# Kernel tuning notes

Hardware: AMD Instinct MI355X
Metric: run time of the kernel (lower is better)

Reference implementation:

```python
import jax, jax.numpy as jnp
import numpy as np

D = 128          # node_embed_size
N_NODES = 100000
E = 600000       # edges per relation (3 relations)
NEG_SLOPE = 0.01 # F.leaky_relu default


def setup_inputs() -> dict:
    key = jax.random.key(0)
    ks = jax.random.split(key, 17)
    s = 1.0 / np.sqrt(D)
    inp = {
        "N": jax.random.normal(ks[0], (N_NODES, D), jnp.float32),
        # fc1 weights per domain: [D, D] (torch Linear weight layout: out x in)
        "W1_0": jax.random.normal(ks[1], (D, D), jnp.float32) * s,
        "W1_1": jax.random.normal(ks[2], (D, D), jnp.float32) * s,
        "W1_2": jax.random.normal(ks[3], (D, D), jnp.float32) * s,
        # fc2 weights per domain: [1, 2D]
        "w2_0": jax.random.normal(ks[4], (1, 2 * D), jnp.float32) * s,
        "w2_1": jax.random.normal(ks[5], (1, 2 * D), jnp.float32) * s,
        "w2_2": jax.random.normal(ks[6], (1, 2 * D), jnp.float32) * s,
        "Wq": jax.random.normal(ks[7], (D, D), jnp.float32) * s,
        "Wk": jax.random.normal(ks[8], (D, D), jnp.float32) * s,
        "Wv": jax.random.normal(ks[9], (D, D), jnp.float32) * s,
        "src0": jax.random.randint(ks[10], (E,), 0, N_NODES, jnp.int32),
        "dst0": jax.random.randint(ks[11], (E,), 0, N_NODES, jnp.int32),
        "src1": jax.random.randint(ks[12], (E,), 0, N_NODES, jnp.int32),
        "dst1": jax.random.randint(ks[13], (E,), 0, N_NODES, jnp.int32),
        "src2": jax.random.randint(ks[14], (E,), 0, N_NODES, jnp.int32),
        "dst2": jax.random.randint(ks[15], (E,), 0, N_NODES, jnp.int32),
        "target_idx": 0,
    }
    return inp


def _leaky(x):
    return jnp.where(x >= 0, x, NEG_SLOPE * x)


def _gat_relation(N, W1, w2, src, dst, n_nodes):
    # e_edge = leaky_relu(fc2(cat(fc1(N[src]), fc1(N[dst]))))
    # fc2 on a concat == left half dot src part + right half dot dst part,
    # so compute per-node scores once and gather (standard GAT trick).
    d = N.shape[1]
    h = N @ W1.T                      # [n, d]
    sl = h @ w2[0, :d]                # [n]
    sr = h @ w2[0, d:]                # [n]
    e = _leaky(sl[src] + sr[dst])     # [E]
    # segment softmax over edges grouped by destination node (DGL mailbox softmax)
    m = jax.ops.segment_max(e, dst, num_segments=n_nodes)   # [n], -inf for empty
    ex = jnp.exp(e - m[dst])                                 # [E]
    den = jax.ops.segment_sum(ex, dst, num_segments=n_nodes) # [n]
    alpha = ex / den[dst]                                    # [E]
    # weighted sum of source features; zero for nodes with no in-edges
    return jax.ops.segment_sum(alpha[:, None] * N[src], dst, num_segments=n_nodes)


def reference(N, W1_0, W1_1, W1_2, w2_0, w2_1, w2_2, Wq, Wk, Wv,
              src0, dst0, src1, dst1, src2, dst2, target_idx):
    n, d = N.shape
    rels = [(W1_0, w2_0, src0, dst0), (W1_1, w2_1, src1, dst1), (W1_2, w2_2, src2, dst2)]
    h = [_gat_relation(N, W1, w2, src, dst, n) for (W1, w2, src, dst) in rels]
    hs = jnp.stack(h)                         # [3, n, d]
    q = h[target_idx] @ Wq.T                  # [n, d]
    k = jnp.einsum('knd,ed->kne', hs, Wk)     # [3, n, d]
    # (Wv value is computed in the original but never used in the output)
    e = jnp.einsum('nd,knd->nk', q, k) / jnp.sqrt(jnp.asarray(d, N.dtype))  # [n, 3]
    a = jax.nn.softmax(e, axis=1)             # [n, 3]
    Np = jnp.einsum('nk,knd->nd', a, hs)      # [n, d]
    return Np
```

## Files before the change

kernel.cpp:

```cpp
#include <hip/hip_runtime.h>
#include <hip/hip_bf16.h>
#include <math.h>

#define DD 128

typedef __attribute__((ext_vector_type(8))) short short8;
typedef __attribute__((ext_vector_type(4))) float f32x4;

static __device__ __forceinline__ unsigned short f2bf(float f) {
    unsigned u = __float_as_uint(f);
    u += 0x7fffu + ((u >> 16) & 1u);
    return (unsigned short)(u >> 16);
}
static __device__ __forceinline__ float bflo(unsigned mm) { return __uint_as_float(mm << 16); }
static __device__ __forceinline__ float bfhi(unsigned mm) { return __uint_as_float(mm & 0xffff0000u); }

static __device__ __forceinline__ f32x4 MFMA(short8 a, short8 b, f32x4 c) {
    return __builtin_amdgcn_mfma_f32_16x16x32_bf16(a, b, c, 0, 0, 0);
}
static __device__ __forceinline__ int uswz(int u) { return u ^ ((u >> 4) & 7); }

__global__ void k_fill(float* __restrict__ out, float v, int n) {
    int i = blockIdx.x * 256 + threadIdx.x;
    if (i < n) out[i] = v;
}

__global__ void k_prep(const float* __restrict__ Wq, const float* __restrict__ Wk,
                       const float* __restrict__ W10, const float* __restrict__ W11,
                       const float* __restrict__ W12,
                       const float* __restrict__ w20, const float* __restrict__ w21,
                       const float* __restrict__ w22,
                       unsigned short* __restrict__ Bh, unsigned short* __restrict__ Bl,
                       float* __restrict__ uv, unsigned* __restrict__ cnt, int SEG) {
    int b = blockIdx.x, j = threadIdx.x;
    if (b < DD) {
        float acc = 0.f;
        for (int k = 0; k < DD; ++k)
            acc += Wq[k*DD + b] * Wk[k*DD + j];
        unsigned short hi = f2bf(acc);
        unsigned short lo = f2bf(acc - bflo(hi));
        int t  = j >> 4;
        int ks = b >> 5;
        int l  = ((b >> 3) & 3) * 16 + (j & 15);
        int jj = b & 7;
        int idx = ((t*4 + ks)*64 + l)*8 + jj;
        Bh[idx] = hi;
        Bl[idx] = lo;
    } else if (b < DD + 3) {
        int r = b - DD;
        const float* W1 = (r==0) ? W10 : (r==1 ? W11 : W12);
        const float* w2 = (r==0) ? w20 : (r==1 ? w21 : w22);
        float u = 0.f, v = 0.f;
        for (int k = 0; k < DD; ++k) {
            float w = W1[k*DD + j];
            u += w2[k]      * w;
            v += w2[DD + k] * w;
        }
        uv[r*256 + j]      = u;
        uv[r*256 + DD + j] = v;
    } else {
        int idx = (b - (DD + 3)) * DD + j;
        if (idx < SEG) cnt[idx] = 0u;
    }
}

__global__ void __launch_bounds__(256) k_scores(
        const float* __restrict__ N, const float* __restrict__ uv,
        float* __restrict__ sl, float* __restrict__ sr,
        uint2* __restrict__ Nbf, unsigned* __restrict__ cnt,
        unsigned* __restrict__ rank,
        const int* __restrict__ d0, const int* __restrict__ d1,
        const int* __restrict__ d2,
        int n, int E) {
    int tid = threadIdx.x;
    int g = blockIdx.x * 256 + tid;
    if (g < 3*E) {
        int r = (g >= 2*E) ? 2 : (g >= E ? 1 : 0);
        int e = g - r*E;
        const int* Dd = (r==0) ? d0 : (r==1 ? d1 : d2);
        rank[g] = atomicAdd(&cnt[(size_t)r*n + Dd[e]], 1u);
    }
    int wave = tid >> 6, lane = tid & 63, half = lane >> 5, l32 = lane & 31;
    int iw = blockIdx.x * 8 + wave * 2 + half;
    if (iw >= n && blockIdx.x * 8 >= n) return;
    int i = (iw < n) ? iw : (n - 1);
    float4 nv = ((const float4*)N)[(size_t)i * 32 + l32];
    if (iw < n) {
        uint2 pk;
        pk.x = (unsigned)f2bf(nv.x) | ((unsigned)f2bf(nv.y) << 16);
        pk.y = (unsigned)f2bf(nv.z) | ((unsigned)f2bf(nv.w) << 16);
        Nbf[(size_t)iw * 32 + l32] = pk;
    }
    const float4* UV4 = (const float4*)uv;
    float acc[6];
#pragma unroll
    for (int r = 0; r < 3; ++r) {
        float4 u = UV4[r*64 + l32];
        float4 v = UV4[r*64 + 32 + l32];
        acc[2*r]   = nv.x*u.x + nv.y*u.y + nv.z*u.z + nv.w*u.w;
        acc[2*r+1] = nv.x*v.x + nv.y*v.y + nv.z*v.z + nv.w*v.w;
    }
#pragma unroll
    for (int o = 16; o; o >>= 1) {
#pragma unroll
        for (int q = 0; q < 6; ++q) acc[q] += __shfl_xor(acc[q], o);
    }
    if (l32 == 0 && iw < n) {
#pragma unroll
        for (int r = 0; r < 3; ++r) {
            sl[(size_t)r*n + iw] = acc[2*r];
            sr[(size_t)r*n + iw] = acc[2*r+1];
        }
    }
}

__global__ void __launch_bounds__(256) k_scan1(unsigned* __restrict__ off,
                                               unsigned* __restrict__ bsum, int SEG) {
    __shared__ unsigned s[256];
    int tid = threadIdx.x;
    int i = blockIdx.x * 256 + tid;
    unsigned v = (i < SEG) ? off[i] : 0u;
    s[tid] = v; __syncthreads();
#pragma unroll
    for (int o = 1; o < 256; o <<= 1) {
        unsigned a = (tid >= o) ? s[tid - o] : 0u; __syncthreads();
        s[tid] += a; __syncthreads();
    }
    if (i < SEG) off[i] = s[tid] - v;
    if (tid == 255) bsum[blockIdx.x] = s[255];
}

__global__ void __launch_bounds__(256) k_scan2(unsigned* __restrict__ bsum, int nb) {
    __shared__ unsigned s[256];
    __shared__ unsigned carry;
    int tid = threadIdx.x;
    if (tid == 0) carry = 0u;
    for (int base = 0; base < nb; base += 256) {
        int i = base + tid;
        unsigned v = (i < nb) ? bsum[i] : 0u;
        __syncthreads();
        s[tid] = v; __syncthreads();
#pragma unroll
        for (int o = 1; o < 256; o <<= 1) {
            unsigned a = (tid >= o) ? s[tid - o] : 0u; __syncthreads();
            s[tid] += a; __syncthreads();
        }
        unsigned incl = s[tid], tot = s[255], c = carry;
        if (i < nb) bsum[i] = c + incl - v;
        __syncthreads();
        if (tid == 0) carry = c + tot;
    }
}

__global__ void k_scatter(const int* __restrict__ s0, const int* __restrict__ d0,
                          const int* __restrict__ s1, const int* __restrict__ d1,
                          const int* __restrict__ s2, const int* __restrict__ d2,
                          const float* __restrict__ sl, const float* __restrict__ sr,
                          const unsigned* __restrict__ off,
                          const unsigned* __restrict__ bsum,
                          const unsigned* __restrict__ rank,
                          uint2* __restrict__ edat, int n, int E) {
    int g = blockIdx.x * 256 + threadIdx.x;
    if (g >= 3*E) return;
    int r = (g >= 2*E) ? 2 : (g >= E ? 1 : 0);
    int e = g - r*E;
    const int* S  = (r==0) ? s0 : (r==1 ? s1 : s2);
    const int* Dd = (r==0) ? d0 : (r==1 ? d1 : d2);
    int si = S[e], di = Dd[e];
    int seg = r*n + di;
    float x = sl[(size_t)r*n + si] + sr[seg];
    x = (x >= 0.f) ? x : 0.01f * x;
    unsigned p = off[seg] + bsum[seg >> 8] + rank[g];
    edat[p] = make_uint2((unsigned)si, __float_as_uint(x));
}

__global__ void __launch_bounds__(256, 8) k_node(
        const uint4* __restrict__ Nbf,
        const uint4* __restrict__ B4h, const uint4* __restrict__ B4l,
        const unsigned* __restrict__ off,
        const unsigned* __restrict__ bsum,
        const uint2* __restrict__ edat,
        const int* __restrict__ tgt,
        float* __restrict__ out, int n, int TOT) {
    __shared__ uint4 afrag[2][256];
    __shared__ float Tl[16*132];
    int tid = threadIdx.x;
    int wave = tid >> 6, lane = tid & 63;
    int grp = lane >> 4;
    int l16 = lane & 15;
    int nid = wave * 4 + grp;
    int iw = blockIdx.x * 16 + nid;
    int i = (iw < n) ? iw : (n - 1);
    int t = tgt[0];
    t = (t < 0) ? 0 : (t > 2 ? 2 : t);
    int SEG = 3*n;

    int A[3], C[3];
#pragma unroll
    for (int r = 0; r < 3; ++r) {
        int seg = r*n + i;
        int a = (int)(off[seg] + bsum[seg >> 8]);
        int b = (seg + 1 < SEG) ? (int)(off[seg+1] + bsum[(seg+1) >> 8]) : TOT;
        A[r] = a; C[r] = b - a;
    }

    float m_[3], inv_[3];
#pragma unroll
    for (int r = 0; r < 3; ++r) {
        int cc = C[r];
        float m, s;
        if (cc <= 16) {
            float x = (l16 < cc) ? __uint_as_float(edat[A[r] + l16].y) : -INFINITY;
            m = x;
#pragma unroll
            for (int o = 8; o; o >>= 1) m = fmaxf(m, __shfl_xor(m, o));
            s = (l16 < cc) ? __expf(x - m) : 0.f;
#pragma unroll
            for (int o = 8; o; o >>= 1) s += __shfl_xor(s, o);
        } else {
            m = -INFINITY;
            for (int j = A[r] + l16; j < A[r] + cc; j += 16)
                m = fmaxf(m, __uint_as_float(edat[j].y));
#pragma unroll
            for (int o = 8; o; o >>= 1) m = fmaxf(m, __shfl_xor(m, o));
            s = 0.f;
            for (int j = A[r] + l16; j < A[r] + cc; j += 16)
                s += __expf(__uint_as_float(edat[j].y) - m);
#pragma unroll
            for (int o = 8; o; o >>= 1) s += __shfl_xor(s, o);
        }
        m_[r] = m; inv_[r] = 1.f / s;
    }

    float hr[3][8];
#pragma unroll
    for (int r = 0; r < 3; ++r) {
        float h[8] = {0.f,0.f,0.f,0.f,0.f,0.f,0.f,0.f};
        int cc = C[r], a = A[r];
        float mm = m_[r], iv = inv_[r];
        for (int p = 0; p < cc; p += 2) {
            int e1 = (p + 1 < cc) ? p + 1 : cc - 1;
            uint2 d0 = edat[a + p];
            uint2 d1 = edat[a + e1];
            uint4 v0 = Nbf[(size_t)d0.x * 16 + l16];
            uint4 v1 = Nbf[(size_t)d1.x * 16 + l16];
            float a0 = __expf(__uint_as_float(d0.y) - mm) * iv;
            float a1 = (p + 1 < cc)
                ? __expf(__uint_as_float(d1.y) - mm) * iv : 0.f;
            h[0] += a0*bflo(v0.x) + a1*bflo(v1.x);
            h[1] += a0*bfhi(v0.x) + a1*bfhi(v1.x);
            h[2] += a0*bflo(v0.y) + a1*bflo(v1.y);
            h[3] += a0*bfhi(v0.y) + a1*bfhi(v1.y);
            h[4] += a0*bflo(v0.z) + a1*bflo(v1.z);
            h[5] += a0*bfhi(v0.z) + a1*bfhi(v1.z);
            h[6] += a0*bflo(v0.w) + a1*bflo(v1.w);
            h[7] += a0*bfhi(v0.w) + a1*bfhi(v1.w);
        }
#pragma unroll
        for (int k = 0; k < 8; ++k) hr[r][k] = h[k];
        if (r == t) {
            unsigned ph[4], pl[4];
#pragma unroll
            for (int k = 0; k < 4; ++k) {
                unsigned short h0 = f2bf(h[2*k]);
                unsigned short h1 = f2bf(h[2*k+1]);
                unsigned short g0 = f2bf(h[2*k]   - bflo(h0));
                unsigned short g1 = f2bf(h[2*k+1] - bflo(h1));
                ph[k] = (unsigned)h0 | ((unsigned)h1 << 16);
                pl[k] = (unsigned)g0 | ((unsigned)g1 << 16);
            }
            int u = uswz(((l16 >> 2) * 64) + ((l16 & 3) * 16) + nid);
            afrag[0][u] = make_uint4(ph[0], ph[1], ph[2], ph[3]);
            afrag[1][u] = make_uint4(pl[0], pl[1], pl[2], pl[3]);
        }
    }
    __syncthreads();

    {
        int qm = lane >> 4;
        f32x4 acc0 = {0.f, 0.f, 0.f, 0.f};
        f32x4 acc1 = {0.f, 0.f, 0.f, 0.f};
        int jt0 = wave*2, jt1 = wave*2 + 1;
        for (int ks = 0; ks < 4; ++ks) {
            uint4 a_hi = afrag[0][uswz(ks*64 + lane)];
            uint4 a_lo = afrag[1][uswz(ks*64 + lane)];
            uint4 b0h = B4h[(jt0*4 + ks)*64 + lane];
            uint4 b0l = B4l[(jt0*4 + ks)*64 + lane];
            uint4 b1h = B4h[(jt1*4 + ks)*64 + lane];
            uint4 b1l = B4l[(jt1*4 + ks)*64 + lane];
            acc0 = MFMA(__builtin_bit_cast(short8, a_hi),
                        __builtin_bit_cast(short8, b0h), acc0);
            acc1 = MFMA(__builtin_bit_cast(short8, a_hi),
                        __builtin_bit_cast(short8, b1h), acc1);
            acc0 = MFMA(__builtin_bit_cast(short8, a_lo),
                        __builtin_bit_cast(short8, b0h), acc0);
            acc1 = MFMA(__builtin_bit_cast(short8, a_lo),
                        __builtin_bit_cast(short8, b1h), acc1);
            acc0 = MFMA(__builtin_bit_cast(short8, a_hi),
                        __builtin_bit_cast(short8, b0l), acc0);
            acc1 = MFMA(__builtin_bit_cast(short8, a_hi),
                        __builtin_bit_cast(short8, b1l), acc1);
        }
        int col0 = jt0*16 + l16, col1 = jt1*16 + l16;
#pragma unroll
        for (int rg = 0; rg < 4; ++rg) {
            Tl[(qm*4 + rg)*132 + col0] = acc0[rg];
            Tl[(qm*4 + rg)*132 + col1] = acc1[rg];
        }
    }
    __syncthreads();

    float4 ta = *(const float4*)&Tl[nid*132 + 8*l16];
    float4 tb = *(const float4*)&Tl[nid*132 + 8*l16 + 4];
    float t8[8] = {ta.x, ta.y, ta.z, ta.w, tb.x, tb.y, tb.z, tb.w};

    const float inv = 0.088388347648318447f;
    float e[3];
#pragma unroll
    for (int r = 0; r < 3; ++r) {
        float v = 0.f;
#pragma unroll
        for (int k = 0; k < 8; ++k) v += t8[k]*hr[r][k];
#pragma unroll
        for (int o = 8; o; o >>= 1) v += __shfl_xor(v, o);
        e[r] = v * inv;
    }
    float mx = fmaxf(e[0], fmaxf(e[1], e[2]));
    float x0 = __expf(e[0]-mx), x1 = __expf(e[1]-mx), x2 = __expf(e[2]-mx);
    float sinv = 1.f / (x0 + x1 + x2);
    float aw0 = x0*sinv, aw1 = x1*sinv, aw2 = x2*sinv;
    if (iw < n) {
        float4 oa, ob;
        oa.x = aw0*hr[0][0] + aw1*hr[1][0] + aw2*hr[2][0];
        oa.y = aw0*hr[0][1] + aw1*hr[1][1] + aw2*hr[2][1];
        oa.z = aw0*hr[0][2] + aw1*hr[1][2] + aw2*hr[2][2];
        oa.w = aw0*hr[0][3] + aw1*hr[1][3] + aw2*hr[2][3];
        ob.x = aw0*hr[0][4] + aw1*hr[1][4] + aw2*hr[2][4];
        ob.y = aw0*hr[0][5] + aw1*hr[1][5] + aw2*hr[2][5];
        ob.z = aw0*hr[0][6] + aw1*hr[1][6] + aw2*hr[2][6];
        ob.w = aw0*hr[0][7] + aw1*hr[1][7] + aw2*hr[2][7];
        ((float4*)(out + (size_t)iw * DD))[2*l16]     = oa;
        ((float4*)(out + (size_t)iw * DD))[2*l16 + 1] = ob;
    }
}

extern "C" void kernel_launch(void* const* d_in, const int* in_sizes, int n_in,
                              void* d_out, int out_size, void* d_ws, size_t ws_size,
                              hipStream_t stream) {
    float* outp = (float*)d_out;
    int fillgrid = (out_size + 255) / 256;
    if (n_in != 17) {
        k_fill<<<fillgrid, 256, 0, stream>>>(outp, 1024.0f, out_size);
        return;
    }
    int n = in_sizes[0] / DD;
    int E = in_sizes[10];
    bool ok = (in_sizes[0] % DD == 0)
        && in_sizes[1]==DD*DD && in_sizes[2]==DD*DD && in_sizes[3]==DD*DD
        && in_sizes[4]==2*DD  && in_sizes[5]==2*DD  && in_sizes[6]==2*DD
        && in_sizes[7]==DD*DD && in_sizes[8]==DD*DD && in_sizes[9]==DD*DD
        && in_sizes[11]==E && in_sizes[12]==E && in_sizes[13]==E
        && in_sizes[14]==E && in_sizes[15]==E && in_sizes[16]==1;
    if (!ok) {
        k_fill<<<fillgrid, 256, 0, stream>>>(outp, 512.0f, out_size);
        return;
    }
    int SEG = 3*n;
    int NB1 = (SEG + 255) / 256;
    int tot = 3*E;

    size_t o_edat = (size_t)2*SEG + 768 + DD*DD + SEG + NB1 + (size_t)tot;
    o_edat = (o_edat + 1) & ~(size_t)1;
    size_t o_nbf = o_edat + (size_t)2*tot;
    o_nbf = (o_nbf + 3) & ~(size_t)3;
    size_t need_f = o_nbf + (size_t)n*64;
    if (ws_size < need_f * sizeof(float)) {
        k_fill<<<fillgrid, 256, 0, stream>>>(outp, 256.0f, out_size);
        return;
    }

    const float* N   = (const float*)d_in[0];
    const float* W10 = (const float*)d_in[1];
    const float* W11 = (const float*)d_in[2];
    const float* W12 = (const float*)d_in[3];
    const float* w20 = (const float*)d_in[4];
    const float* w21 = (const float*)d_in[5];
    const float* w22 = (const float*)d_in[6];
    const float* Wq  = (const float*)d_in[7];
    const float* Wk  = (const float*)d_in[8];
    const int* s0 = (const int*)d_in[10];
    const int* d0 = (const int*)d_in[11];
    const int* s1 = (const int*)d_in[12];
    const int* d1 = (const int*)d_in[13];
    const int* s2 = (const int*)d_in[14];
    const int* d2 = (const int*)d_in[15];
    const int* tgt = (const int*)d_in[16];

    float* ws = (float*)d_ws;
    float* sl = ws;
    float* sr = sl + SEG;
    float* uv = sr + SEG;
    unsigned short* Bh = (unsigned short*)(uv + 768);
    unsigned short* Bl = Bh + DD*DD;
    unsigned* off  = (unsigned*)(uv + 768 + DD*DD);
    unsigned* bsum = off + SEG;
    unsigned* rank = bsum + NB1;
    uint2*    edat = (uint2*)(ws + o_edat);
    unsigned* Nbf  = (unsigned*)(ws + o_nbf);

    int NBZ = (SEG + DD - 1) / DD;
    int gridS = (n + 7) / 8;
    int gridC = (tot + 255) / 256;
    if (gridC > gridS) gridS = gridC;

    k_prep<<<DD + 3 + NBZ, DD, 0, stream>>>(Wq, Wk, W10, W11, W12,
                                            w20, w21, w22, Bh, Bl, uv, off, SEG);
    k_scores<<<gridS, 256, 0, stream>>>(N, uv, sl, sr, (uint2*)Nbf, off, rank,
                                        d0, d1, d2, n, E);
    k_scan1<<<NB1, 256, 0, stream>>>(off, bsum, SEG);
    k_scan2<<<1, 256, 0, stream>>>(bsum, NB1);
    k_scatter<<<(tot + 255)/256, 256, 0, stream>>>(s0,d0,s1,d1,s2,d2, sl,sr,
                                                   off, bsum, rank, edat, n, E);
    k_node<<<(n + 15)/16, 256, 0, stream>>>((const uint4*)Nbf,
                                            (const uint4*)Bh, (const uint4*)Bl,
                                            off, bsum, edat, tgt, outp, n, tot);
}
```

Measured before the change: 388.1 us.

## Fuse front-end kernels into one cooperative persistent kernel with grid syncs

Replaces the five front-end launches (prep, scores/counting, two scan passes, scatter) with a single cooperative kernel of 1024 blocks that uses grid-stride loops and grid-wide syncs between phases. This removes per-launch overhead and the pipeline drain between small kernels. In exchange, the grid barriers and the single-block second scan serialise work, and the fixed grid may underuse or oversubscribe the device. Cooperative launch also requires every block to be co-resident, with occupancy limited by launch_bounds(256,4).

```diff
diff --git a/kernel.cpp b/kernel.cpp
--- a/kernel.cpp
+++ b/kernel.cpp
@@ -1,8 +1,11 @@
 #include <hip/hip_runtime.h>
 #include <hip/hip_bf16.h>
+#include <hip/hip_cooperative_groups.h>
 #include <math.h>
 
 #define DD 128
+
+namespace cg = cooperative_groups;
 
 typedef __attribute__((ext_vector_type(8))) short short8;
 typedef __attribute__((ext_vector_type(4))) float f32x4;
@@ -25,29 +28,48 @@
     if (i < n) out[i] = v;
 }
 
-__global__ void k_prep(const float* __restrict__ Wq, const float* __restrict__ Wk,
-                       const float* __restrict__ W10, const float* __restrict__ W11,
-                       const float* __restrict__ W12,
-                       const float* __restrict__ w20, const float* __restrict__ w21,
-                       const float* __restrict__ w22,
-                       unsigned short* __restrict__ Bh, unsigned short* __restrict__ Bl,
-                       float* __restrict__ uv, unsigned* __restrict__ cnt, int SEG) {
-    int b = blockIdx.x, j = threadIdx.x;
-    if (b < DD) {
+__global__ void __launch_bounds__(256, 4) k_front(
+        const float* __restrict__ N,
+        const float* __restrict__ Wq, const float* __restrict__ Wk,
+        const float* __restrict__ W10, const float* __restrict__ W11,
+        const float* __restrict__ W12,
+        const float* __restrict__ w20, const float* __restrict__ w21,
+        const float* __restrict__ w22,
+        const int* __restrict__ s0, const int* __restrict__ d0,
+        const int* __restrict__ s1, const int* __restrict__ d1,
+        const int* __restrict__ s2, const int* __restrict__ d2,
+        unsigned short* __restrict__ Bh, unsigned short* __restrict__ Bl,
+        float* __restrict__ uv, float* __restrict__ sl, float* __restrict__ sr,
+        uint2* __restrict__ Nbf, unsigned* __restrict__ off,
+        unsigned* __restrict__ bsum, unsigned* __restrict__ rank,
+        uint2* __restrict__ edat,
+        int n, int E) {
+    cg::grid_group gg = cg::this_grid();
+    __shared__ unsigned smem[256];
+    __shared__ unsigned carry;
+    int tid = threadIdx.x, bid = blockIdx.x, nb = gridDim.x;
+    int gsz = nb * 256, g0 = bid * 256 + tid;
+    int SEG = 3*n;
+    int NB1 = (SEG + 255) >> 8;
+    int tot3 = 3*E;
+
+    for (int idx = g0; idx < DD*DD; idx += gsz) {
+        int c = idx >> 7, j = idx & 127;
         float acc = 0.f;
         for (int k = 0; k < DD; ++k)
-            acc += Wq[k*DD + b] * Wk[k*DD + j];
+            acc += Wq[k*DD + c] * Wk[k*DD + j];
         unsigned short hi = f2bf(acc);
         unsigned short lo = f2bf(acc - bflo(hi));
         int t  = j >> 4;
-        int ks = b >> 5;
-        int l  = ((b >> 3) & 3) * 16 + (j & 15);
-        int jj = b & 7;
-        int idx = ((t*4 + ks)*64 + l)*8 + jj;
-        Bh[idx] = hi;
-        Bl[idx] = lo;
-    } else if (b < DD + 3) {
-        int r = b - DD;
+        int ks = c >> 5;
+        int l  = ((c >> 3) & 3) * 16 + (j & 15);
+        int jj = c & 7;
+        int fidx = ((t*4 + ks)*64 + l)*8 + jj;
+        Bh[fidx] = hi;
+        Bl[fidx] = lo;
+    }
+    for (int idx = g0; idx < 3*DD; idx += gsz) {
+        int r = idx >> 7, j = idx & 127;
         const float* W1 = (r==0) ? W10 : (r==1 ? W11 : W12);
         const float* w2 = (r==0) ? w20 : (r==1 ? w21 : w22);
         float u = 0.f, v = 0.f;
@@ -58,120 +80,101 @@
         }
         uv[r*256 + j]      = u;
         uv[r*256 + DD + j] = v;
-    } else {
-        int idx = (b - (DD + 3)) * DD + j;
-        if (idx < SEG) cnt[idx] = 0u;
-    }
-}
-
-__global__ void __launch_bounds__(256) k_scores(
-        const float* __restrict__ N, const float* __restrict__ uv,
-        float* __restrict__ sl, float* __restrict__ sr,
-        uint2* __restrict__ Nbf, unsigned* __restrict__ cnt,
-        unsigned* __restrict__ rank,
-        const int* __restrict__ d0, const int* __restrict__ d1,
-        const int* __restrict__ d2,
-        int n, int E) {
-    int tid = threadIdx.x;
-    int g = blockIdx.x * 256 + tid;
-    if (g < 3*E) {
+    }
+    for (int idx = g0; idx < SEG; idx += gsz) off[idx] = 0u;
+    gg.sync();
+
+    for (int g = g0; g < tot3; g += gsz) {
         int r = (g >= 2*E) ? 2 : (g >= E ? 1 : 0);
         int e = g - r*E;
         const int* Dd = (r==0) ? d0 : (r==1 ? d1 : d2);
-        rank[g] = atomicAdd(&cnt[(size_t)r*n + Dd[e]], 1u);
-    }
-    int wave = tid >> 6, lane = tid & 63, half = lane >> 5, l32 = lane & 31;
-    int iw = blockIdx.x * 8 + wave * 2 + half;
-    if (iw >= n && blockIdx.x * 8 >= n) return;
-    int i = (iw < n) ? iw : (n - 1);
-    float4 nv = ((const float4*)N)[(size_t)i * 32 + l32];
-    if (iw < n) {
-        uint2 pk;
-        pk.x = (unsigned)f2bf(nv.x) | ((unsigned)f2bf(nv.y) << 16);
-        pk.y = (unsigned)f2bf(nv.z) | ((unsigned)f2bf(nv.w) << 16);
-        Nbf[(size_t)iw * 32 + l32] = pk;
-    }
-    const float4* UV4 = (const float4*)uv;
-    float acc[6];
-#pragma unroll
-    for (int r = 0; r < 3; ++r) {
-        float4 u = UV4[r*64 + l32];
-        float4 v = UV4[r*64 + 32 + l32];
-        acc[2*r]   = nv.x*u.x + nv.y*u.y + nv.z*u.z + nv.w*u.w;
-        acc[2*r+1] = nv.x*v.x + nv.y*v.y + nv.z*v.z + nv.w*v.w;
-    }
-#pragma unroll
-    for (int o = 16; o; o >>= 1) {
-#pragma unroll
-        for (int q = 0; q < 6; ++q) acc[q] += __shfl_xor(acc[q], o);
-    }
-    if (l32 == 0 && iw < n) {
-#pragma unroll
-        for (int r = 0; r < 3; ++r) {
-            sl[(size_t)r*n + iw] = acc[2*r];
-            sr[(size_t)r*n + iw] = acc[2*r+1];
-        }
-    }
-}
-
-__global__ void __launch_bounds__(256) k_scan1(unsigned* __restrict__ off,
-                                               unsigned* __restrict__ bsum, int SEG) {
-    __shared__ unsigned s[256];
-    int tid = threadIdx.x;
-    int i = blockIdx.x * 256 + tid;
-    unsigned v = (i < SEG) ? off[i] : 0u;
-    s[tid] = v; __syncthreads();
-#pragma unroll
-    for (int o = 1; o < 256; o <<= 1) {
-        unsigned a = (tid >= o) ? s[tid - o] : 0u; __syncthreads();
-        s[tid] += a; __syncthreads();
-    }
-    if (i < SEG) off[i] = s[tid] - v;
-    if (tid == 255) bsum[blockIdx.x] = s[255];
-}
-
-__global__ void __launch_bounds__(256) k_scan2(unsigned* __restrict__ bsum, int nb) {
-    __shared__ unsigned s[256];
-    __shared__ unsigned carry;
-    int tid = threadIdx.x;
-    if (tid == 0) carry = 0u;
-    for (int base = 0; base < nb; base += 256) {
-        int i = base + tid;
-        unsigned v = (i < nb) ? bsum[i] : 0u;
+        rank[g] = atomicAdd(&off[(size_t)r*n + Dd[e]], 1u);
+    }
+    {
+        int wave = tid >> 6, lane = tid & 63, half = lane >> 5, l32 = lane & 31;
+        int ntile = (n + 7) >> 3;
+        const float4* UV4 = (const float4*)uv;
+        for (int ib = bid; ib < ntile; ib += nb) {
+            int iw = ib*8 + wave*2 + half;
+            int i = (iw < n) ? iw : (n - 1);
+            float4 nv = ((const float4*)N)[(size_t)i * 32 + l32];
+            if (iw < n) {
+                uint2 pk;
+                pk.x = (unsigned)f2bf(nv.x) | ((unsigned)f2bf(nv.y) << 16);
+                pk.y = (unsigned)f2bf(nv.z) | ((unsigned)f2bf(nv.w) << 16);
+                Nbf[(size_t)iw * 32 + l32] = pk;
+            }
+            float acc[6];
+#pragma unroll
+            for (int r = 0; r < 3; ++r) {
+                float4 u = UV4[r*64 + l32];
+                float4 v = UV4[r*64 + 32 + l32];
+                acc[2*r]   = nv.x*u.x + nv.y*u.y + nv.z*u.z + nv.w*u.w;
+                acc[2*r+1] = nv.x*v.x + nv.y*v.y + nv.z*v.z + nv.w*v.w;
+            }
+#pragma unroll
+            for (int o = 16; o; o >>= 1) {
+#pragma unroll
+                for (int q = 0; q < 6; ++q) acc[q] += __shfl_xor(acc[q], o);
+            }
+            if (l32 == 0 && iw < n) {
+#pragma unroll
+                for (int r = 0; r < 3; ++r) {
+                    sl[(size_t)r*n + iw] = acc[2*r];
+                    sr[(size_t)r*n + iw] = acc[2*r+1];
+                }
+            }
+        }
+    }
+    gg.sync();
+
+    for (int tb = bid; tb < NB1; tb += nb) {
+        int i = tb*256 + tid;
+        unsigned v = (i < SEG) ? off[i] : 0u;
+        smem[tid] = v; __syncthreads();
+#pragma unroll
+        for (int o = 1; o < 256; o <<= 1) {
+            unsigned a = (tid >= o) ? smem[tid - o] : 0u; __syncthreads();
+            smem[tid] += a; __syncthreads();
+        }
+        if (i < SEG) off[i] = smem[tid] - v;
+        if (tid == 255) bsum[tb] = smem[255];
         __syncthreads();
-        s[tid] = v; __syncthreads();
-#pragma unroll
-        for (int o = 1; o < 256; o <<= 1) {
-            unsigned a = (tid >= o) ? s[tid - o] : 0u; __syncthreads();
-            s[tid] += a; __syncthreads();
-        }
-        unsigned incl = s[tid], tot = s[255], c = carry;
-        if (i < nb) bsum[i] = c + incl - v;
-        __syncthreads();
-        if (tid == 0) carry = c + tot;
-    }
-}
-
-__global__ void k_scatter(const int* __restrict__ s0, const int* __restrict__ d0,
-                          const int* __restrict__ s1, const int* __restrict__ d1,
-                          const int* __restrict__ s2, const int* __restrict__ d2,
-                          const float* __restrict__ sl, const float* __restrict__ sr,
-                          const unsigned* __restrict__ off,
-                          const unsigned* __restrict__ bsum,
-                          const unsigned* __restrict__ rank,
-                          uint2* __restrict__ edat, int n, int E) {
-    int g = blockIdx.x * 256 + threadIdx.x;
-    if (g >= 3*E) return;
-    int r = (g >= 2*E) ? 2 : (g >= E ? 1 : 0);
-    int e = g - r*E;
-    const int* S  = (r==0) ? s0 : (r==1 ? s1 : s2);
-    const int* Dd = (r==0) ? d0 : (r==1 ? d1 : d2);
-    int si = S[e], di = Dd[e];
-    int seg = r*n + di;
-    float x = sl[(size_t)r*n + si] + sr[seg];
-    x = (x >= 0.f) ? x : 0.01f * x;
-    unsigned p = off[seg] + bsum[seg >> 8] + rank[g];
-    edat[p] = make_uint2((unsigned)si, __float_as_uint(x));
+    }
+    gg.sync();
+
+    if (bid == 0) {
+        if (tid == 0) carry = 0u;
+        for (int base = 0; base < NB1; base += 256) {
+            int i = base + tid;
+            unsigned v = (i < NB1) ? bsum[i] : 0u;
+            __syncthreads();
+            smem[tid] = v; __syncthreads();
+#pragma unroll
+            for (int o = 1; o < 256; o <<= 1) {
+                unsigned a = (tid >= o) ? smem[tid - o] : 0u; __syncthreads();
+                smem[tid] += a; __syncthreads();
+            }
+            unsigned incl = smem[tid], tt = smem[255], c = carry;
+            if (i < NB1) bsum[i] = c + incl - v;
+            __syncthreads();
+            if (tid == 0) carry = c + tt;
+        }
+    }
+    gg.sync();
+
+    for (int g = g0; g < tot3; g += gsz) {
+        int r = (g >= 2*E) ? 2 : (g >= E ? 1 : 0);
+        int e = g - r*E;
+        const int* S  = (r==0) ? s0 : (r==1 ? s1 : s2);
+        const int* Dd = (r==0) ? d0 : (r==1 ? d1 : d2);
+        int si = S[e], di = Dd[e];
+        int seg = r*n + di;
+        float x = sl[(size_t)r*n + si] + sr[seg];
+        x = (x >= 0.f) ? x : 0.01f * x;
+        unsigned p = off[seg] + bsum[seg >> 8] + rank[g];
+        edat[p] = make_uint2((unsigned)si, __float_as_uint(x));
+    }
 }
 
 __global__ void __launch_bounds__(256, 8) k_node(
@@ -406,21 +409,23 @@
     unsigned* bsum = off + SEG;
     unsigned* rank = bsum + NB1;
     uint2*    edat = (uint2*)(ws + o_edat);
-    unsigned* Nbf  = (unsigned*)(ws + o_nbf);
-
-    int NBZ = (SEG + DD - 1) / DD;
-    int gridS = (n + 7) / 8;
-    int gridC = (tot + 255) / 256;
-    if (gridC > gridS) gridS = gridC;
-
-    k_prep<<<DD + 3 + NBZ, DD, 0, stream>>>(Wq, Wk, W10, W11, W12,
-                                            w20, w21, w22, Bh, Bl, uv, off, SEG);
-    k_scores<<<gridS, 256, 0, stream>>>(N, uv, sl, sr, (uint2*)Nbf, off, rank,
-                                        d0, d1, d2, n, E);
-    k_scan1<<<NB1, 256, 0, stream>>>(off, bsum, SEG);
-    k_scan2<<<1, 256, 0, stream>>>(bsum, NB1);
-    k_scatter<<<(tot + 255)/256, 256, 0, stream>>>(s0,d0,s1,d1,s2,d2, sl,sr,
-                                                   off, bsum, rank, edat, n, E);
+    uint2*    Nbf  = (uint2*)(ws + o_nbf);
+
+    {
+        int nn = n, EE = E;
+        void* args[] = {
+            (void*)&N, (void*)&Wq, (void*)&Wk,
+            (void*)&W10, (void*)&W11, (void*)&W12,
+            (void*)&w20, (void*)&w21, (void*)&w22,
+            (void*)&s0, (void*)&d0, (void*)&s1, (void*)&d1,
+            (void*)&s2, (void*)&d2,
+            (void*)&Bh, (void*)&Bl, (void*)&uv, (void*)&sl, (void*)&sr,
+            (void*)&Nbf, (void*)&off, (void*)&bsum, (void*)&rank,
+            (void*)&edat, (void*)&nn, (void*)&EE
+        };
+        hipLaunchCooperativeKernel((void*)k_front, dim3(1024), dim3(256),
+                                   args, 0, stream);
+    }
     k_node<<<(n + 15)/16, 256, 0, stream>>>((const uint4*)Nbf,
                                             (const uint4*)Bh, (const uint4*)Bl,
                                             off, bsum, edat, tgt, outp, n, tot);
```

Result: slower. 828.3 us (+113.4%).

## Replace two-pass scan with single-pass decoupled look-back and unroll edge gather

Applied to the files above, without the earlier changes.

Replaces the two-kernel block-sum scan with a single-pass decoupled look-back scan that writes absolute offsets directly, so the scatter and node kernels no longer add a block-sum term. It also unrolls the per-node edge aggregation loop from 2 to 4 edges per iteration to expose more independent gather loads. The look-back depends on blocks making forward progress in launch order, and the zeroing region is extended to cover the descriptor array. The wider unroll raises register pressure in the node kernel.

```diff
diff --git a/kernel.cpp b/kernel.cpp
--- a/kernel.cpp
+++ b/kernel.cpp
@@ -31,7 +31,7 @@
                        const float* __restrict__ w20, const float* __restrict__ w21,
                        const float* __restrict__ w22,
                        unsigned short* __restrict__ Bh, unsigned short* __restrict__ Bl,
-                       float* __restrict__ uv, unsigned* __restrict__ cnt, int SEG) {
+                       float* __restrict__ uv, unsigned* __restrict__ cnt, int NZ) {
     int b = blockIdx.x, j = threadIdx.x;
     if (b < DD) {
         float acc = 0.f;
@@ -60,7 +60,7 @@
         uv[r*256 + DD + j] = v;
     } else {
         int idx = (b - (DD + 3)) * DD + j;
-        if (idx < SEG) cnt[idx] = 0u;
+        if (idx < NZ) cnt[idx] = 0u;
     }
 }
 
@@ -114,6 +114,43 @@
     }
 }
 
+__global__ void __launch_bounds__(256, 8) k_scan(unsigned* __restrict__ off,
+                                                 unsigned* __restrict__ desc,
+                                                 int SEG) {
+    __shared__ unsigned s[256];
+    __shared__ unsigned pfx;
+    int tid = threadIdx.x, b = blockIdx.x;
+    int i = b * 256 + tid;
+    unsigned v = (i < SEG) ? off[i] : 0u;
+    s[tid] = v; __syncthreads();
+#pragma unroll
+    for (int o = 1; o < 256; o <<= 1) {
+        unsigned a = (tid >= o) ? s[tid - o] : 0u; __syncthreads();
+        s[tid] += a; __syncthreads();
+    }
+    unsigned excl = s[tid] - v, tt = s[255];
+    if (tid == 0) {
+        if (b == 0) {
+            atomicExch(&desc[0], 0x80000000u | tt);
+            pfx = 0u;
+        } else {
+            atomicExch(&desc[b], 0x40000000u | tt);
+            unsigned run = 0u; int j = b - 1;
+            for (;;) {
+                unsigned d;
+                do { d = atomicAdd(&desc[j], 0u); } while (d == 0u);
+                run += d & 0x3FFFFFFFu;
+                if (d & 0x80000000u) break;
+                --j;
+            }
+            atomicExch(&desc[b], 0x80000000u | ((run + tt) & 0x3FFFFFFFu));
+            pfx = run;
+        }
+    }
+    __syncthreads();
+    if (i < SEG) off[i] = excl + pfx;
+}
+
 __global__ void __launch_bounds__(256) k_scan1(unsigned* __restrict__ off,
                                                unsigned* __restrict__ bsum, int SEG) {
     __shared__ unsigned s[256];
@@ -129,7 +166,6 @@
     if (i < SEG) off[i] = s[tid] - v;
     if (tid == 255) bsum[blockIdx.x] = s[255];
 }
-
 __global__ void __launch_bounds__(256) k_scan2(unsigned* __restrict__ bsum, int nb) {
     __shared__ unsigned s[256];
     __shared__ unsigned carry;
@@ -151,13 +187,17 @@
         if (tid == 0) carry = c + tot;
     }
 }
+__global__ void k_absoff(unsigned* __restrict__ off,
+                         const unsigned* __restrict__ bsum, int SEG) {
+    int i = blockIdx.x * 256 + threadIdx.x;
+    if (i < SEG) off[i] += bsum[i >> 8];
+}
 
 __global__ void k_scatter(const int* __restrict__ s0, const int* __restrict__ d0,
                           const int* __restrict__ s1, const int* __restrict__ d1,
                           const int* __restrict__ s2, const int* __restrict__ d2,
                           const float* __restrict__ sl, const float* __restrict__ sr,
                           const unsigned* __restrict__ off,
-                          const unsigned* __restrict__ bsum,
                           const unsigned* __restrict__ rank,
                           uint2* __restrict__ edat, int n, int E) {
     int g = blockIdx.x * 256 + threadIdx.x;
@@ -170,7 +210,7 @@
     int seg = r*n + di;
     float x = sl[(size_t)r*n + si] + sr[seg];
     x = (x >= 0.f) ? x : 0.01f * x;
-    unsigned p = off[seg] + bsum[seg >> 8] + rank[g];
+    unsigned p = off[seg] + rank[g];
     edat[p] = make_uint2((unsigned)si, __float_as_uint(x));
 }
 
@@ -178,7 +218,6 @@
         const uint4* __restrict__ Nbf,
         const uint4* __restrict__ B4h, const uint4* __restrict__ B4l,
         const unsigned* __restrict__ off,
-        const unsigned* __restrict__ bsum,
         const uint2* __restrict__ edat,
         const int* __restrict__ tgt,
         float* __restrict__ out, int n, int TOT) {
@@ -199,8 +238,8 @@
 #pragma unroll
     for (int r = 0; r < 3; ++r) {
         int seg = r*n + i;
-        int a = (int)(off[seg] + bsum[seg >> 8]);
-        int b = (seg + 1 < SEG) ? (int)(off[seg+1] + bsum[(seg+1) >> 8]) : TOT;
+        int a = (int)off[seg];
+        int b = (seg + 1 < SEG) ? (int)off[seg+1] : TOT;
         A[r] = a; C[r] = b - a;
     }
 
@@ -238,23 +277,30 @@
         float h[8] = {0.f,0.f,0.f,0.f,0.f,0.f,0.f,0.f};
         int cc = C[r], a = A[r];
         float mm = m_[r], iv = inv_[r];
-        for (int p = 0; p < cc; p += 2) {
+        for (int p = 0; p < cc; p += 4) {
             int e1 = (p + 1 < cc) ? p + 1 : cc - 1;
+            int e2 = (p + 2 < cc) ? p + 2 : cc - 1;
+            int e3 = (p + 3 < cc) ? p + 3 : cc - 1;
             uint2 d0 = edat[a + p];
             uint2 d1 = edat[a + e1];
+            uint2 d2 = edat[a + e2];
+            uint2 d3 = edat[a + e3];
             uint4 v0 = Nbf[(size_t)d0.x * 16 + l16];
             uint4 v1 = Nbf[(size_t)d1.x * 16 + l16];
+            uint4 v2 = Nbf[(size_t)d2.x * 16 + l16];
+            uint4 v3 = Nbf[(size_t)d3.x * 16 + l16];
             float a0 = __expf(__uint_as_float(d0.y) - mm) * iv;
-            float a1 = (p + 1 < cc)
-                ? __expf(__uint_as_float(d1.y) - mm) * iv : 0.f;
-            h[0] += a0*bflo(v0.x) + a1*bflo(v1.x);
-            h[1] += a0*bfhi(v0.x) + a1*bfhi(v1.x);
-            h[2] += a0*bflo(v0.y) + a1*bflo(v1.y);
-            h[3] += a0*bfhi(v0.y) + a1*bfhi(v1.y);
-            h[4] += a0*bflo(v0.z) + a1*bflo(v1.z);
-            h[5] += a0*bfhi(v0.z) + a1*bfhi(v1.z);
-            h[6] += a0*bflo(v0.w) + a1*bflo(v1.w);
-            h[7] += a0*bfhi(v0.w) + a1*bfhi(v1.w);
+            float a1 = (p + 1 < cc) ? __expf(__uint_as_float(d1.y) - mm) * iv : 0.f;
+            float a2 = (p + 2 < cc) ? __expf(__uint_as_float(d2.y) - mm) * iv : 0.f;
+            float a3 = (p + 3 < cc) ? __expf(__uint_as_float(d3.y) - mm) * iv : 0.f;
+            h[0] += a0*bflo(v0.x) + a1*bflo(v1.x) + a2*bflo(v2.x) + a3*bflo(v3.x);
+            h[1] += a0*bfhi(v0.x) + a1*bfhi(v1.x) + a2*bfhi(v2.x) + a3*bfhi(v3.x);
+            h[2] += a0*bflo(v0.y) + a1*bflo(v1.y) + a2*bflo(v2.y) + a3*bflo(v3.y);
+            h[3] += a0*bfhi(v0.y) + a1*bfhi(v1.y) + a2*bfhi(v2.y) + a3*bfhi(v3.y);
+            h[4] += a0*bflo(v0.z) + a1*bflo(v1.z) + a2*bflo(v2.z) + a3*bflo(v3.z);
+            h[5] += a0*bfhi(v0.z) + a1*bfhi(v1.z) + a2*bfhi(v2.z) + a3*bfhi(v3.z);
+            h[6] += a0*bflo(v0.w) + a1*bflo(v1.w) + a2*bflo(v2.w) + a3*bflo(v3.w);
+            h[7] += a0*bfhi(v0.w) + a1*bfhi(v1.w) + a2*bfhi(v2.w) + a3*bfhi(v3.w);
         }
 #pragma unroll
         for (int k = 0; k < 8; ++k) hr[r][k] = h[k];
@@ -403,25 +449,31 @@
     unsigned short* Bh = (unsigned short*)(uv + 768);
     unsigned short* Bl = Bh + DD*DD;
     unsigned* off  = (unsigned*)(uv + 768 + DD*DD);
-    unsigned* bsum = off + SEG;
-    unsigned* rank = bsum + NB1;
+    unsigned* desc = off + SEG;
+    unsigned* rank = desc + NB1;
     uint2*    edat = (uint2*)(ws + o_edat);
     unsigned* Nbf  = (unsigned*)(ws + o_nbf);
 
-    int NBZ = (SEG + DD - 1) / DD;
+    int NZ  = SEG + NB1;
+    int NBZ = (NZ + DD - 1) / DD;
     int gridS = (n + 7) / 8;
     int gridC = (tot + 255) / 256;
     if (gridC > gridS) gridS = gridC;
 
     k_prep<<<DD + 3 + NBZ, DD, 0, stream>>>(Wq, Wk, W10, W11, W12,
-                                            w20, w21, w22, Bh, Bl, uv, off, SEG);
+                                            w20, w21, w22, Bh, Bl, uv, off, NZ);
     k_scores<<<gridS, 256, 0, stream>>>(N, uv, sl, sr, (uint2*)Nbf, off, rank,
                                         d0, d1, d2, n, E);
-    k_scan1<<<NB1, 256, 0, stream>>>(off, bsum, SEG);
-    k_scan2<<<1, 256, 0, stream>>>(bsum, NB1);
+    if (NB1 <= 2000) {
+        k_scan<<<NB1, 256, 0, stream>>>(off, desc, SEG);
+    } else {
+        k_scan1<<<NB1, 256, 0, stream>>>(off, desc, SEG);
+        k_scan2<<<1, 256, 0, stream>>>(desc, NB1);
+        k_absoff<<<NB1, 256, 0, stream>>>(off, desc, SEG);
+    }
     k_scatter<<<(tot + 255)/256, 256, 0, stream>>>(s0,d0,s1,d1,s2,d2, sl,sr,
-                                                   off, bsum, rank, edat, n, E);
+                                                   off, rank, edat, n, E);
     k_node<<<(n + 15)/16, 256, 0, stream>>>((const uint4*)Nbf,
                                             (const uint4*)Bh, (const uint4*)Bl,
-                                            off, bsum, edat, tgt, outp, n, tot);
-}
+                                            off, edat, tgt, outp, n, tot);
+}
```

Result: slower. 471.4 us (+21.5%).
